# Kernel tuning notes

Measured on AMD Instinct MI355X. Metric: run time of the kernel, lower is better.

The kernel has to match this reference:

```python
import jax, jax.numpy as jnp
import numpy as np
from jax import lax

B, N, S, P, FIN, FFUT, H, NB, TOPK = 4, 1437, 56, 28, 10, 6, 64, 2, 5


def layer_norm(x, g, b, eps=1e-5):
    m = x.mean(-1, keepdims=True)
    v = ((x - m) ** 2).mean(-1, keepdims=True)
    return (x - m) * lax.rsqrt(v + eps) * g + b


def conv1d_same(x, w, pl, pr):
    # x: [BNF, 1, S], w: [1, 1, k]; torch Conv1d is cross-correlation == XLA conv
    return lax.conv_general_dilated(x, w, (1,), [(pl, pr)], dimension_numbers=('NCH', 'OIH', 'NCH'))


def gelu(x):
    return jax.nn.gelu(x, approximate=False)


def mixer_block(x, adj, wk, mk, lcg, lcb, ltg, ltb, lfg, lfb, lsg, lsb, tw, tb, fw, fb, sw, sb):
    Bx, Nx, Sx, Fx = x.shape
    # conv branch (pre-norm)
    xn = layer_norm(x, lcg, lcb)
    xc = xn.transpose(0, 1, 3, 2).reshape(Bx * Nx * Fx, 1, Sx)
    weekly = conv1d_same(xc, wk, 3, 3).reshape(Bx, Nx, Fx, Sx).transpose(0, 1, 3, 2)
    monthly = conv1d_same(xc, mk, 13, 14).reshape(Bx, Nx, Fx, Sx).transpose(0, 1, 3, 2)
    x = x + weekly + monthly
    # temporal MLP over S
    xn = layer_norm(x, ltg, ltb)
    xt = gelu(jnp.einsum('bnfs,os->bnfo', xn.transpose(0, 1, 3, 2), tw) + tb)
    x = x + xt.transpose(0, 1, 3, 2)
    # feature MLP over Feat
    xn = layer_norm(x, lfg, lfb)
    x = x + gelu(jnp.einsum('bnsf,of->bnso', xn, fw) + fb)
    # spatial propagation via dense bmm with adj
    xn = layer_norm(x, lsg, lsb)
    xp = jnp.einsum('bnsf,of->bnso', xn, sw).reshape(Bx, Nx, Sx * Fx)
    xs = jnp.einsum('bmn,bnd->bmd', adj, xp).reshape(Bx, Nx, Sx, Fx) + sb
    return x + xs


def reference(x, x_future, adj, fp_w, fp_b, in_ln_g, in_ln_b, q_w, q_b, k_w, k_b,
              node_emb, graph_alpha, blk_weekly, blk_monthly,
              blk_lnc_g, blk_lnc_b, blk_lnt_g, blk_lnt_b, blk_lnf_g, blk_lnf_b,
              blk_lns_g, blk_lns_b, blk_temp_w, blk_temp_b, blk_feat_w, blk_feat_b,
              blk_spat_w, blk_spat_b, futr_w, futr_b, head_w, head_b):
    Bx, Nx, Sx, _ = x.shape
    h = jnp.einsum('bnsf,hf->bnsh', x, fp_w) + fp_b
    h = layer_norm(h, in_ln_g, in_ln_b)
    emb = node_emb / jnp.maximum(jnp.linalg.norm(node_emb, axis=-1, keepdims=True), 1e-12)
    h = h + emb[None, :, None, :]
    # recency-weighted context
    decay = jnp.exp(-jnp.arange(Sx, 0, -1, dtype=jnp.float32) / 14.0)
    rw = decay / decay.sum()
    ctx = (h * rw[None, None, :, None]).sum(2)  # [B,N,H]
    Q = ctx @ q_w.T + q_b
    K = ctx @ k_w.T + k_b
    da = jnp.einsum('bnh,bmh->bnm', Q, K) / jnp.sqrt(jnp.float32(Q.shape[-1]))
    da = jax.nn.relu(jnp.clip(da, -10.0, 10.0))
    _, ti = lax.top_k(da, TOPK)
    mask = jax.vmap(jax.vmap(lambda row, idx: row.at[idx].set(1.0)))(
        jnp.zeros((Bx, Nx, Nx), da.dtype), ti)
    dyn = jax.nn.softmax(jnp.where(mask > 0, da, -jnp.inf), axis=2)
    dyn = jnp.nan_to_num(dyn)
    alpha = jax.nn.sigmoid(graph_alpha)  # shape (1,), broadcasts
    comb = alpha * adj[None, :, :] + (1.0 - alpha) * dyn
    comb = comb / jnp.maximum(jnp.abs(comb).sum(axis=2, keepdims=True), 1e-12)
    for i in range(NB):
        h = mixer_block(h, comb, blk_weekly[i], blk_monthly[i],
                        blk_lnc_g[i], blk_lnc_b[i], blk_lnt_g[i], blk_lnt_b[i],
                        blk_lnf_g[i], blk_lnf_b[i], blk_lns_g[i], blk_lns_b[i],
                        blk_temp_w[i], blk_temp_b[i], blk_feat_w[i], blk_feat_b[i],
                        blk_spat_w[i], blk_spat_b[i])
    hist = h.reshape(Bx, Nx, -1)
    fut = (jnp.einsum('bnpf,hf->bnph', x_future, futr_w) + futr_b).reshape(Bx, Nx, -1)
    feats = jnp.concatenate([hist, fut], axis=2)
    return feats @ head_w.T + head_b


def setup_inputs() -> dict:
    key = jax.random.key(0)
    ks = jax.random.split(key, 16)
    rn = lambda k, shp, s=1.0: jax.random.normal(k, shp, dtype=jnp.float32) * s
    return {
        'x': rn(ks[0], (B, N, S, FIN)),
        'x_future': rn(ks[1], (B, N, P, FFUT)),
        'adj': jax.random.uniform(ks[2], (N, N), dtype=jnp.float32),
        'fp_w': rn(ks[3], (H, FIN), 0.1), 'fp_b': jnp.zeros((H,), jnp.float32),
        'in_ln_g': jnp.ones((H,), jnp.float32), 'in_ln_b': jnp.zeros((H,), jnp.float32),
        'q_w': rn(ks[4], (H, H), 0.1), 'q_b': jnp.zeros((H,), jnp.float32),
        'k_w': rn(ks[5], (H, H), 0.1), 'k_b': jnp.zeros((H,), jnp.float32),
        'node_emb': rn(ks[6], (N, H), 0.02),
        'graph_alpha': jnp.full((1,), 2.2, jnp.float32),
        'blk_weekly': rn(ks[7], (NB, 1, 1, 7), 0.1),
        'blk_monthly': rn(ks[8], (NB, 1, 1, 28), 0.1),
        'blk_lnc_g': jnp.ones((NB, H), jnp.float32), 'blk_lnc_b': jnp.zeros((NB, H), jnp.float32),
        'blk_lnt_g': jnp.ones((NB, H), jnp.float32), 'blk_lnt_b': jnp.zeros((NB, H), jnp.float32),
        'blk_lnf_g': jnp.ones((NB, H), jnp.float32), 'blk_lnf_b': jnp.zeros((NB, H), jnp.float32),
        'blk_lns_g': jnp.ones((NB, H), jnp.float32), 'blk_lns_b': jnp.zeros((NB, H), jnp.float32),
        'blk_temp_w': rn(ks[9], (NB, S, S), 0.1), 'blk_temp_b': jnp.zeros((NB, S), jnp.float32),
        'blk_feat_w': rn(ks[10], (NB, H, H), 0.1), 'blk_feat_b': jnp.zeros((NB, H), jnp.float32),
        'blk_spat_w': rn(ks[11], (NB, H, H), 0.1), 'blk_spat_b': jnp.zeros((NB, H), jnp.float32),
        'futr_w': rn(ks[12], (H, FFUT), 0.1), 'futr_b': jnp.zeros((H,), jnp.float32),
        'head_w': rn(ks[13], (P, S * H + P * H), 0.02), 'head_b': jnp.zeros((P,), jnp.float32),
    }
```

## Files before the change

kernel.cpp:

```cpp
#include <hip/hip_runtime.h>
#include <hip/hip_bf16.h>
#include <math.h>

#define BB 4
#define NN 1437
#define SS 56
#define PP 28
#define FIN 10
#define FFUT 6
#define HH 64
#define NBLK 2
#define TOPK 5
#define DD (SS*HH)
#define FD (PP*HH)
#define TOT (DD+FD)
#define MP 1536
#define KP 1472
#define NT (KP/32)
#define WIMG_SZ 16384

typedef __attribute__((ext_vector_type(8))) __bf16 bf16x8;
typedef __attribute__((ext_vector_type(4))) float  f32x4;


__device__ __forceinline__ float gelu_fast(float x){
    float x2 = x*x;
    float u  = __builtin_fmaf(0.044715f*x2, x, x);
    float e  = __builtin_amdgcn_exp2f(2.3022077f*u);
    float r  = __builtin_amdgcn_rcpf(e+1.f);
    return x - x*r;
}
template<int C>
__device__ __forceinline__ float dppadd(float v){
    int x = __builtin_amdgcn_mov_dpp(__float_as_int(v), C, 0xF, 0xF, true);
    return v + __int_as_float(x);
}
__device__ __forceinline__ float row16_sum(float v){
    v = dppadd<0xB1>(v);
    v = dppadd<0x4E>(v);
    v = dppadd<0x141>(v);
    v = dppadd<0x140>(v);
    return v;
}
__device__ __forceinline__ float wave_sum64(float v){
    v = row16_sum(v);
    v += __shfl_xor(v,16,64);
    v += __shfl_xor(v,32,64);
    return v;
}
__device__ __forceinline__ void async_load16(const void* g, void* l){
    __builtin_amdgcn_global_load_lds(
        (const __attribute__((address_space(1))) void*)g,
        (__attribute__((address_space(3))) void*)l, 16, 0, 0);
}
__device__ __forceinline__ unsigned short f2bf(float x){
    unsigned int u = __float_as_uint(x);
    unsigned int r = (u + 0x7fffu + ((u>>16)&1u)) >> 16;
    return (unsigned short)r;
}
__device__ __forceinline__ float bf2f(unsigned short u){
    return __uint_as_float(((unsigned int)u)<<16);
}
__device__ __forceinline__ unsigned long long umax64(unsigned long long a, unsigned long long b){return a>b?a:b;}
__device__ __forceinline__ unsigned long long umin64(unsigned long long a, unsigned long long b){return a<b?a:b;}

#define INS5(a0,a1,a2,a3,a4,x) do{ unsigned long long t_=(x); \
    unsigned long long n0_=umax64(a0,t_), t1_=umin64(a0,t_); \
    unsigned long long n1_=umax64(a1,t1_), t2_=umin64(a1,t1_); \
    unsigned long long n2_=umax64(a2,t2_), t3_=umin64(a2,t2_); \
    unsigned long long n3_=umax64(a3,t3_), t4_=umin64(a3,t3_); \
    unsigned long long n4_=umax64(a4,t4_); \
    a0=n0_;a1=n1_;a2=n2_;a3=n3_;a4=n4_; }while(0)

#define MERGE5(a0,a1,a2,a3,a4,b0,b1,b2,b3,b4) do{ \
    unsigned long long o0_=umax64(a0,(b0)); \
    unsigned long long o1_=umax64(umax64((b1),umin64(a0,(b0))),a1); \
    unsigned long long o2_=umax64(umax64((b2),umin64(a0,(b1))),umax64(umin64(a1,(b0)),a2)); \
    unsigned long long o3_=umax64(umax64((b3),umin64(a0,(b2))),umax64(umin64(a1,(b1)),umax64(umin64(a2,(b0)),a3))); \
    unsigned long long o4_=umax64(umax64((b4),umin64(a0,(b3))),umax64(umax64(umin64(a1,(b2)),umin64(a2,(b1))),umax64(umin64(a3,(b0)),a4))); \
    a0=o0_;a1=o1_;a2=o2_;a3=o3_;a4=o4_; }while(0)

__global__ __launch_bounds__(256) void k_front(
    const float* __restrict__ x, const float* __restrict__ fpw, const float* __restrict__ fpb,
    const float* __restrict__ lng, const float* __restrict__ lnb,
    const float* __restrict__ nemb,
    const float* __restrict__ qw, const float* __restrict__ qb,
    const float* __restrict__ kw, const float* __restrict__ kb,
    float* __restrict__ h,
    unsigned short* __restrict__ qpack, unsigned short* __restrict__ kpack)
{
    int bn = blockIdx.x; int n = bn % NN;
    int tid=threadIdx.x; int lane=tid&63; int wv=tid>>6;
    __shared__ float xin[SS*FIN];
    __shared__ float wlds[HH*FIN];
    __shared__ float rw[SS];
    __shared__ float rsum;
    __shared__ float red[4][HH];
    __shared__ float ctxs[HH];
    for (int i=tid;i<SS*FIN;i+=256) xin[i]=x[(size_t)bn*SS*FIN+i];
    for (int i=tid;i<HH*FIN;i+=256) wlds[i]=fpw[i];
    if (tid<SS) rw[tid]=expf(-(float)(SS-tid)/14.0f);
    __syncthreads();
    if (tid==0){ float s=0.f; for(int i=0;i<SS;++i) s+=rw[i]; rsum=s; }
    __syncthreads();
    float inv_rs = 1.0f/rsum;
    float ev = nemb[(size_t)n*HH+lane];
    float ss = wave_sum64(ev*ev);
    float el = ev / fmaxf(sqrtf(ss), 1e-12f);
    float gg=lng[lane], bv=lnb[lane], fb0=fpb[lane];
    int paddr = (lane&15)*4 + (lane>>4);
    float cacc=0.f;
    for (int s=wv;s<SS;s+=4){
        float v=fb0;
        #pragma unroll
        for (int c=0;c<FIN;++c) v += xin[s*FIN+c]*wlds[lane*FIN+c];
        float m = wave_sum64(v)*(1.f/HH);
        float d = v-m;
        float va = wave_sum64(d*d)*(1.f/HH);
        float hn = d*rsqrtf(va+1e-5f)*gg + bv + el;
        h[((size_t)bn*SS+s)*HH + paddr]=hn;
        cacc += hn * rw[s]*inv_rs;
    }
    red[wv][lane]=cacc;
    __syncthreads();
    if (wv==0) ctxs[lane]=red[0][lane]+red[1][lane]+red[2][lane]+red[3][lane];
    __syncthreads();
    if (wv==0){
        const float4* qr = reinterpret_cast<const float4*>(qw + (size_t)lane*HH);
        const float4* kr = reinterpret_cast<const float4*>(kw + (size_t)lane*HH);
        float q=qb[lane], k=kb[lane];
        #pragma unroll 4
        for (int t=0;t<16;++t){
            float4 qv=qr[t], kv=kr[t];
            float c0=ctxs[4*t], c1=ctxs[4*t+1], c2=ctxs[4*t+2], c3=ctxs[4*t+3];
            q += qv.x*c0+qv.y*c1+qv.z*c2+qv.w*c3;
            k += kv.x*c0+kv.y*c1+kv.z*c2+kv.w*c3;
        }
        int b = bn/NN, m = bn%NN;
        size_t off = (size_t)b*8*MP*8 + (size_t)(lane>>3)*MP*8 + (size_t)m*8 + (lane&7);
        qpack[off]=f2bf(q); kpack[off]=f2bf(k);
    }
}

__global__ __launch_bounds__(256) void k_adjsum(
    const float* __restrict__ adj, float* __restrict__ adjsum)
{
    int m = blockIdx.x*4 + (threadIdx.x>>6);
    int lane = threadIdx.x & 63;
    if (m >= NN) return;
    const float* row = adj + (size_t)m*NN;
    float s=0.f;
    for (int n=lane;n<NN;n+=64) s += row[n];
    s = wave_sum64(s);
    if (lane==0) adjsum[m]=s;
}

__global__ __launch_bounds__(256) void k_qkt_top5(
    const unsigned short* __restrict__ qp, const unsigned short* __restrict__ kp,
    const float* __restrict__ adjsum, const float* __restrict__ galpha,
    int* __restrict__ meta_idx, float* __restrict__ meta_p, float* __restrict__ meta_inv)
{
    int m0 = blockIdx.x*32; int b = blockIdx.y;
    int tid=threadIdx.x, lane=tid&63, w=tid>>6;
    int g=lane>>4, c15=lane&15;
    int wr=w>>1, wc=w&1;
    __shared__ unsigned long long mls[64][5];

    const unsigned short* qb2 = qp + (size_t)b*8*MP*8;
    const unsigned short* kb2 = kp + (size_t)b*8*MP*8;
    bf16x8 af0 = *(const bf16x8*)(qb2 + ((size_t)(0*4+g)*MP + m0+wr*16+c15)*8);
    bf16x8 af1 = *(const bf16x8*)(qb2 + ((size_t)(1*4+g)*MP + m0+wr*16+c15)*8);

    unsigned long long A0=0,A1=0,A2=0,A3=0,A4=0;
    unsigned long long B0=0,B1=0,B2=0,B3=0,B4=0;
    unsigned long long C0=0,C1=0,C2=0,C3=0,C4=0;
    unsigned long long D0=0,D1=0,D2=0,D3=0,D4=0;

    for (int t=0;t<12;++t){
        int n0 = t*128;
        f32x4 acc[4];
        #pragma unroll
        for (int j=0;j<4;++j) acc[j]=(f32x4){0.f,0.f,0.f,0.f};
        #pragma unroll
        for (int j=0;j<4;++j){
            bf16x8 b0 = *(const bf16x8*)(kb2 + ((size_t)(0*4+g)*MP + n0+wc*64+j*16+c15)*8);
            bf16x8 b1 = *(const bf16x8*)(kb2 + ((size_t)(1*4+g)*MP + n0+wc*64+j*16+c15)*8);
            acc[j]=__builtin_amdgcn_mfma_f32_16x16x32_bf16(af0,b0,acc[j],0,0,0);
            acc[j]=__builtin_amdgcn_mfma_f32_16x16x32_bf16(af1,b1,acc[j],0,0,0);
        }
        #pragma unroll
        for (int j=0;j<4;++j){
            int n = n0 + wc*64 + j*16 + c15;
            bool ok = (n < NN);
            unsigned int lowk = 0xFFFFFFFFu - (unsigned)n;
            #define MKKEY(Q) ({ \
                float v_ = acc[j][Q]*0.125f; \
                v_ = fminf(fmaxf(v_,0.f),10.f); \
                ok ? (((unsigned long long)__float_as_uint(v_)<<32)|(unsigned long long)lowk) : 0ULL; })
            { unsigned long long k_=MKKEY(0); INS5(A0,A1,A2,A3,A4,k_); }
            { unsigned long long k_=MKKEY(1); INS5(B0,B1,B2,B3,B4,k_); }
            { unsigned long long k_=MKKEY(2); INS5(C0,C1,C2,C3,C4,k_); }
            { unsigned long long k_=MKKEY(3); INS5(D0,D1,D2,D3,D4,k_); }
            #undef MKKEY
        }
    }
    #pragma unroll
    for (int off=1; off<16; off<<=1){
        unsigned long long t0,t1,t2,t3,t4;
        t0=__shfl_xor(A0,off,64); t1=__shfl_xor(A1,off,64); t2=__shfl_xor(A2,off,64); t3=__shfl_xor(A3,off,64); t4=__shfl_xor(A4,off,64);
        MERGE5(A0,A1,A2,A3,A4,t0,t1,t2,t3,t4);
        t0=__shfl_xor(B0,off,64); t1=__shfl_xor(B1,off,64); t2=__shfl_xor(B2,off,64); t3=__shfl_xor(B3,off,64); t4=__shfl_xor(B4,off,64);
        MERGE5(B0,B1,B2,B3,B4,t0,t1,t2,t3,t4);
        t0=__shfl_xor(C0,off,64); t1=__shfl_xor(C1,off,64); t2=__shfl_xor(C2,off,64); t3=__shfl_xor(C3,off,64); t4=__shfl_xor(C4,off,64);
        MERGE5(C0,C1,C2,C3,C4,t0,t1,t2,t3,t4);
        t0=__shfl_xor(D0,off,64); t1=__shfl_xor(D1,off,64); t2=__shfl_xor(D2,off,64); t3=__shfl_xor(D3,off,64); t4=__shfl_xor(D4,off,64);
        MERGE5(D0,D1,D2,D3,D4,t0,t1,t2,t3,t4);
    }
    if (c15==0){
        int rb = wr*16 + g*4;
        mls[(rb+0)*2+wc][0]=A0; mls[(rb+0)*2+wc][1]=A1; mls[(rb+0)*2+wc][2]=A2; mls[(rb+0)*2+wc][3]=A3; mls[(rb+0)*2+wc][4]=A4;
        mls[(rb+1)*2+wc][0]=B0; mls[(rb+1)*2+wc][1]=B1; mls[(rb+1)*2+wc][2]=B2; mls[(rb+1)*2+wc][3]=B3; mls[(rb+1)*2+wc][4]=B4;
        mls[(rb+2)*2+wc][0]=C0; mls[(rb+2)*2+wc][1]=C1; mls[(rb+2)*2+wc][2]=C2; mls[(rb+2)*2+wc][3]=C3; mls[(rb+2)*2+wc][4]=C4;
        mls[(rb+3)*2+wc][0]=D0; mls[(rb+3)*2+wc][1]=D1; mls[(rb+3)*2+wc][2]=D2; mls[(rb+3)*2+wc][3]=D3; mls[(rb+3)*2+wc][4]=D4;
    }
    __syncthreads();
    if (tid < 32){
        int m = m0 + tid;
        if (m < NN){
            unsigned long long u0=mls[tid*2][0],u1=mls[tid*2][1],u2=mls[tid*2][2],u3=mls[tid*2][3],u4=mls[tid*2][4];
            MERGE5(u0,u1,u2,u3,u4, mls[tid*2+1][0],mls[tid*2+1][1],mls[tid*2+1][2],mls[tid*2+1][3],mls[tid*2+1][4]);
            float s0=__uint_as_float((unsigned)(u0>>32)), s1=__uint_as_float((unsigned)(u1>>32)),
                  s2=__uint_as_float((unsigned)(u2>>32)), s3=__uint_as_float((unsigned)(u3>>32)),
                  s4=__uint_as_float((unsigned)(u4>>32));
            int i0=(int)(0xFFFFFFFFu-(unsigned)u0), i1=(int)(0xFFFFFFFFu-(unsigned)u1),
                i2=(int)(0xFFFFFFFFu-(unsigned)u2), i3=(int)(0xFFFFFFFFu-(unsigned)u3),
                i4=(int)(0xFFFFFFFFu-(unsigned)u4);
            float e0=1.f, e1=expf(s1-s0), e2=expf(s2-s0), e3=expf(s3-s0), e4=expf(s4-s0);
            float den=e0+e1+e2+e3+e4;
            float alpha=1.f/(1.f+expf(-galpha[0]));
            float oma=(1.f-alpha)/den;
            size_t base = ((size_t)b*NN + m)*5;
            meta_idx[base+0]=i0; meta_idx[base+1]=i1; meta_idx[base+2]=i2; meta_idx[base+3]=i3; meta_idx[base+4]=i4;
            meta_p[base+0]=oma*e0; meta_p[base+1]=oma*e1; meta_p[base+2]=oma*e2; meta_p[base+3]=oma*e3; meta_p[base+4]=oma*e4;
            meta_inv[(size_t)b*NN+m] = 1.f/fmaxf(alpha*adjsum[m] + (1.f-alpha), 1e-12f);
        }
    }
}

__global__ __launch_bounds__(256) void k_blend(
    const float* __restrict__ adj, const float* __restrict__ galpha,
    const int* __restrict__ meta_idx, const float* __restrict__ meta_p,
    const float* __restrict__ meta_inv, __hip_bfloat16* __restrict__ combh)
{
    int m=blockIdx.x, b=blockIdx.y, tid=threadIdx.x;
    size_t base = ((size_t)b*NN + m)*5;
    int i0=meta_idx[base+0], i1=meta_idx[base+1], i2=meta_idx[base+2],
        i3=meta_idx[base+3], i4=meta_idx[base+4];
    float p0=meta_p[base+0], p1=meta_p[base+1], p2=meta_p[base+2],
          p3=meta_p[base+3], p4=meta_p[base+4];
    float inv = meta_inv[(size_t)b*NN+m];
    float alpha=1.f/(1.f+expf(-galpha[0]));
    const float* arow = adj + (size_t)m*NN;
    __hip_bfloat16* dst = combh + ((size_t)b*MP+m)*KP;
    float ai = alpha*inv;
    for (int n=tid;n<KP;n+=256){
        float v = 0.f;
        if (n<NN){
            v = ai*arow[n];
            v += (n==i0)?p0*inv:0.f;
            v += (n==i1)?p1*inv:0.f;
            v += (n==i2)?p2*inv:0.f;
            v += (n==i3)?p3*inv:0.f;
            v += (n==i4)?p4*inv:0.f;
        }
        dst[n]=__float2bfloat16(v);
    }
}

__global__ __launch_bounds__(256) void k_prepw(
    const float* __restrict__ wk, const float* __restrict__ mk,
    const float* __restrict__ tw, const float* __restrict__ fw,
    const float* __restrict__ sw, unsigned short* __restrict__ wimg)
{
    int i = blockIdx.x; int tid = threadIdx.x;
    const float* wki = wk + i*7;
    const float* mki = mk + i*28;
    const float* twi = tw + i*SS*SS;
    const float* fwi = fw + i*HH*HH;
    const float* swi = sw + i*HH*HH;
    unsigned short* o = wimg + (size_t)i*WIMG_SZ;
    for (int e=tid; e<4096; e+=256){
        int r = e>>6, k = e&63;
        int swz = ((k*2) ^ ((r&7)<<4)) >> 1;
        float mv = 0.f;
        if (r<SS && k<SS){
            int a = k-r+3;  if (a>=0 && a<7)  mv += wki[a];
            int b2= k-r+13; if (b2>=0 && b2<28) mv += mki[b2];
        }
        o[r*64 + swz] = f2bf(mv);
        float tv = (r<SS && k<SS) ? twi[r*SS+k] : 0.f;
        o[4096 + r*64 + swz] = f2bf(tv);
        int pk = (k>>3)*512 + r*8 + (k&7);
        o[8192  + pk] = f2bf(fwi[r*HH+k]);
        o[12288 + pk] = f2bf(swi[r*HH+k]);
    }
}

__global__ __launch_bounds__(256) void k_prep_head(
    const float* __restrict__ hw, __hip_bfloat16* __restrict__ hw16)
{
    int i = blockIdx.x*256 + threadIdx.x;
    int r = i / TOT, k = i - r*TOT;
    float v = (r<PP) ? hw[(size_t)r*TOT + k] : 0.f;
    hw16[i] = __float2bfloat16(v);
}

__global__ __launch_bounds__(256) void k_fut(
    const float* __restrict__ xf, const float* __restrict__ fw,
    const float* __restrict__ fbias, __hip_bfloat16* __restrict__ feats)
{
    int bn=blockIdx.x, tid=threadIdx.x;
    __shared__ float fwl[HH*FFUT];
    __shared__ float fbl[HH];
    __shared__ float xfl[PP*FFUT];
    for (int i=tid;i<HH*FFUT;i+=256) fwl[i]=fw[i];
    if (tid<HH) fbl[tid]=fbias[tid];
    for (int i=tid;i<PP*FFUT;i+=256) xfl[i]=xf[(size_t)bn*PP*FFUT+i];
    __syncthreads();
    __hip_bfloat16* dst = feats + (size_t)bn*TOT + DD;
    for (int q=tid;q<FD;q+=256){
        int pp=q>>6, hh2=q&63;
        float v=fbl[hh2];
        #pragma unroll
        for (int c2=0;c2<FFUT;++c2) v += xfl[pp*FFUT+c2]*fwl[hh2*FFUT+c2];
        dst[q]=__float2bfloat16(v);
    }
}

__global__ __launch_bounds__(256) void k_mixer2(
    float* __restrict__ h, unsigned short* __restrict__ xpg,
    const unsigned short* __restrict__ spat_in,
    const unsigned short* __restrict__ wimg,
    const float* __restrict__ lncg, const float* __restrict__ lncb,
    const float* __restrict__ lntg, const float* __restrict__ lntb,
    const float* __restrict__ lnfg, const float* __restrict__ lnfb,
    const float* __restrict__ lnsg, const float* __restrict__ lnsb,
    const float* __restrict__ tb, const float* __restrict__ fb)
{
    int bid = blockIdx.x;
    int xx = bid & 7, ii = bid >> 3;
    int bn = (xx < 4) ? xx*719 + ii : 2876 + (xx-4)*718 + ii;
    int tid=threadIdx.x, lane=tid&63, w=tid>>6;
    int g=lane>>4, c=lane&15;
    __shared__ unsigned short wbuf[2][4096];
    __shared__ unsigned short xs[4096];
    __shared__ float prm[640];

    const char* wsrc=(const char*)wimg;
#define LOADW(SLOTB, BUFP) do{ \
    async_load16(wsrc+(size_t)(SLOTB)+((size_t)tid)*16,       (char*)(BUFP)+(w*64)*16); \
    async_load16(wsrc+(size_t)(SLOTB)+((size_t)(256+tid))*16, (char*)(BUFP)+((256+w*64))*16); } while(0)

    LOADW(0,    wbuf[0]);
    LOADW(8192, wbuf[1]);
    if (tid<64){
        prm[tid]      =lncg[tid]; prm[64+tid] =lncb[tid];
        prm[128+tid]  =lntg[tid]; prm[192+tid]=lntb[tid];
        prm[256+tid]  =lnfg[tid]; prm[320+tid]=lnfb[tid];
        prm[384+tid]  =lnsg[tid]; prm[448+tid]=lnsb[tid];
        prm[512+tid]  =(tid<SS)?tb[tid]:0.f;
        prm[576+tid]  =fb[tid];
    }
    float xl[4][4];
    float* hb = h + (size_t)bn*DD;
    int srow = 16*w + 4*g;
    #pragma unroll
    for (int q=0;q<4;++q){
        int s=srow+q;
        if (s<SS){
            const float4 v4 = *reinterpret_cast<const float4*>(hb + s*HH + c*4);
            float a0=v4.x, a1=v4.y, a2=v4.z, a3=v4.w;
            if (spat_in){
                ushort4 sv = *reinterpret_cast<const ushort4*>(spat_in + (size_t)bn*TOT + s*HH + c*4);
                a0 += bf2f(sv.x); a1 += bf2f(sv.y); a2 += bf2f(sv.z); a3 += bf2f(sv.w);
            }
            xl[q][0]=a0; xl[q][1]=a1; xl[q][2]=a2; xl[q][3]=a3;
        } else {
            xl[q][0]=0.f; xl[q][1]=0.f; xl[q][2]=0.f; xl[q][3]=0.f;
        }
    }
    __syncthreads();

    float xn[4][4];
    f32x4 acc[4];

#define LNSTAGE(GOFF,BOFF) do{ \
    _Pragma("unroll") \
    for (int q=0;q<4;++q){ \
        float sv = xl[q][0]+xl[q][1]+xl[q][2]+xl[q][3]; \
        float s2 = xl[q][0]*xl[q][0]+xl[q][1]*xl[q][1]+xl[q][2]*xl[q][2]+xl[q][3]*xl[q][3]; \
        sv = row16_sum(sv); \
        s2 = row16_sum(s2); \
        float mn = sv*(1.f/64.f); \
        float var = s2*(1.f/64.f)-mn*mn; \
        float rstd = rsqrtf(var+1e-5f); \
        bool ok = (srow+q)<SS; \
        _Pragma("unroll") \
        for (int tj=0;tj<4;++tj){ \
            float v=(xl[q][tj]-mn)*rstd*prm[(GOFF)+tj*16+c]+prm[(BOFF)+tj*16+c]; \
            xn[q][tj]= ok ? v : 0.f; \
        } \
    } }while(0)

#define WRITE_XNP() do{ \
    _Pragma("unroll") \
    for (int qp=0;qp<2;++qp){ \
        int s0=srow+2*qp; \
        _Pragma("unroll") \
        for (int tj=0;tj<4;++tj){ \
            unsigned int pv=(unsigned int)f2bf(xn[2*qp][tj])|((unsigned int)f2bf(xn[2*qp+1][tj])<<16); \
            *(unsigned int*)((char*)xs + ((s0>>3)*1024 + (tj*16+c)*16 + (s0&7)*2)) = pv; \
        } \
    } }while(0)

#define WRITE_XNR() do{ \
    _Pragma("unroll") \
    for (int q=0;q<4;++q){ int s=srow+q; \
        _Pragma("unroll") \
        for (int tj=0;tj<4;++tj){ \
            *(unsigned short*)((char*)xs + s*128 + (((tj*16+c)*2) ^ ((s&7)<<4))) = f2bf(xn[q][tj]); \
        } \
    } }while(0)

#define MM(APTR,BPTR) do{ \
    _Pragma("unroll") \
    for (int tj=0;tj<4;++tj) acc[tj]=(f32x4){0.f,0.f,0.f,0.f}; \
    _Pragma("unroll") \
    for (int kc=0;kc<2;++kc){ \
        int arow=16*w+c; \
        bf16x8 af=*(const bf16x8*)((const char*)(APTR)+arow*128+((kc*64+g*16)^((arow&7)<<4))); \
        _Pragma("unroll") \
        for (int tj=0;tj<4;++tj){ \
            bf16x8 bf2=*(const bf16x8*)((const char*)(BPTR)+(kc*4+g)*1024+(tj*16+c)*16); \
            acc[tj]=__builtin_amdgcn_mfma_f32_16x16x32_bf16(af,bf2,acc[tj],0,0,0); \
        } \
    } }while(0)

    LNSTAGE(0,64); WRITE_XNP();
    __syncthreads();
    MM(&wbuf[0][0], xs);
    #pragma unroll
    for (int q=0;q<4;++q)
        #pragma unroll
        for (int tj=0;tj<4;++tj) xl[q][tj]+=acc[tj][q];
    __syncthreads();
    LOADW(16384, wbuf[0]);
    LNSTAGE(128,192); WRITE_XNP();
    __syncthreads();
    MM(&wbuf[1][0], xs);
    #pragma unroll
    for (int q=0;q<4;++q){
        float tbv=prm[512+srow+q];
        #pragma unroll
        for (int tj=0;tj<4;++tj) xl[q][tj]+=gelu_fast(acc[tj][q]+tbv);
    }
    __syncthreads();
    LOADW(24576, wbuf[1]);
    LNSTAGE(256,320); WRITE_XNR();
    __syncthreads();
    MM(xs, &wbuf[0][0]);
    #pragma unroll
    for (int q=0;q<4;++q)
        #pragma unroll
        for (int tj=0;tj<4;++tj) xl[q][tj]+=gelu_fast(acc[tj][q]+prm[576+tj*16+c]);
    __syncthreads();
    LNSTAGE(384,448); WRITE_XNR();
    __syncthreads();
    MM(xs, &wbuf[1][0]);
    int b_=bn/NN, n_=bn%NN;
    unsigned short* xpo = xpg + ((size_t)b_*(KP/8) + (size_t)(n_>>3))*(size_t)DD*8 + (n_&7);
    #pragma unroll
    for (int q=0;q<4;++q){
        int s=srow+q;
        if (s<SS){
            float4 hv; hv.x=xl[q][0]; hv.y=xl[q][1]; hv.z=xl[q][2]; hv.w=xl[q][3];
            *reinterpret_cast<float4*>(hb + s*HH + c*4) = hv;
            #pragma unroll
            for (int tj=0;tj<4;++tj){
                int d = s*HH + tj*16 + c;
                xpo[(size_t)d*8] = f2bf(acc[tj][q]);
            }
        }
    }
#undef LNSTAGE
#undef WRITE_XNP
#undef WRITE_XNR
#undef MM
#undef LOADW
}

__global__ __launch_bounds__(256,4) void k_bmm_mfma(
    const __hip_bfloat16* __restrict__ combh,
    const __hip_bfloat16* __restrict__ xpg,
    const float* __restrict__ sb,
    const float* __restrict__ h,
    unsigned short* __restrict__ spat_out,
    __hip_bfloat16* __restrict__ feats_out)
{
    __shared__ short As[3][2048];
    __shared__ short Bs[3][4096];

    int bid = blockIdx.x;
    int wg = (bid & 7)*336 + (bid >> 3);
    int bm = wg % 24; int tmp2 = wg / 24; int bd = tmp2 % 28; int b = tmp2 / 28;
    int tid=threadIdx.x, lane=tid&63, w=tid>>6;
    int g=lane>>4, c=lane&15;
    int wr=w>>1, wc=w&1;
    int m0=bm*64, d0=bd*128;

    const char* cb = (const char*)(combh + (size_t)b*MP*KP);
    const char* xb = (const char*)(xpg   + (size_t)b*(KP/8)*(size_t)DD*8);

    int arow_s = tid>>2, aslot = tid&3;
    int ag = aslot ^ ((arow_s>>1)&3);
    const char* srcA = cb + ((size_t)(m0+arow_s)*KP + ag*8)*2;
    int bch = tid>>7, bcol = tid&127;
    const char* srcB0 = xb + ((size_t)bch*DD + d0 + bcol)*16;
    const char* srcB1 = xb + ((size_t)(bch+2)*DD + d0 + bcol)*16;
    const size_t BSTEP = (size_t)4*DD*16;

    f32x4 acc[2][4];
    #pragma unroll
    for (int i=0;i<2;++i)
        #pragma unroll
        for (int j=0;j<4;++j) acc[i][j]=(f32x4){0.f,0.f,0.f,0.f};

    int aoff[2], boff[4];
    #pragma unroll
    for (int i=0;i<2;++i){
        int row = 32*wr + 16*i + c;
        aoff[i] = row*64 + ((g*16) ^ (((row>>1)&3)<<4));
    }
    #pragma unroll
    for (int j=0;j<4;++j) boff[j] = (g*128 + 64*wc + 16*j + c)*16;

#define STAGE(BUF,T) do { \
    async_load16(srcA  + (size_t)(T)*64,    (char*)As[BUF] + w*1024); \
    async_load16(srcB0 + (size_t)(T)*BSTEP, (char*)Bs[BUF] + w*1024); \
    async_load16(srcB1 + (size_t)(T)*BSTEP, (char*)Bs[BUF] + 4096 + w*1024); } while(0)

    STAGE(0,0); STAGE(1,1);
    asm volatile("s_waitcnt vmcnt(3)" ::: "memory");
    __builtin_amdgcn_s_barrier();

    int cur=0;
    for (int t=0;t<NT;++t){
        if (t+2<NT){
            int nb = cur+2; if (nb>=3) nb-=3;
            STAGE(nb, t+2);
        }
        const char* Ab=(const char*)As[cur];
        const char* Bb=(const char*)Bs[cur];
        bf16x8 af[2], bfv[4];
        #pragma unroll
        for (int i=0;i<2;++i) af[i]=*(const bf16x8*)(Ab + aoff[i]);
        #pragma unroll
        for (int j=0;j<4;++j) bfv[j]=*(const bf16x8*)(Bb + boff[j]);
        #pragma unroll
        for (int i=0;i<2;++i)
            #pragma unroll
            for (int j=0;j<4;++j)
                acc[i][j]=__builtin_amdgcn_mfma_f32_16x16x32_bf16(af[i],bfv[j],acc[i][j],0,0,0);
        if (t+2<NT) asm volatile("s_waitcnt vmcnt(3)" ::: "memory");
        else        asm volatile("s_waitcnt vmcnt(0)" ::: "memory");
        __builtin_amdgcn_s_barrier();
        ++cur; if (cur>=3) cur=0;
    }
#undef STAGE

    int row_b = m0 + 32*wr + g*4;
    int s2 = 2*bd + wc;
    float sb0=sb[c], sb1=sb[16+c], sb2=sb[32+c], sb3=sb[48+c];
    #pragma unroll
    for (int i=0;i<2;++i){
        #pragma unroll
        for (int q=0;q<4;++q){
            int m = row_b + 16*i + q;
            if (m < NN){
                if (spat_out){
                    ushort4 pv;
                    pv.x = f2bf(acc[i][0][q] + sb0);
                    pv.y = f2bf(acc[i][1][q] + sb1);
                    pv.z = f2bf(acc[i][2][q] + sb2);
                    pv.w = f2bf(acc[i][3][q] + sb3);
                    *reinterpret_cast<ushort4*>(spat_out + ((size_t)b*NN+m)*TOT + s2*HH + c*4) = pv;
                } else {
                    const float* hp = h + ((size_t)b*NN+m)*DD + s2*HH + c*4;
                    float4 hv = *reinterpret_cast<const float4*>(hp);
                    float nv0 = hv.x + acc[i][0][q] + sb0;
                    float nv1 = hv.y + acc[i][1][q] + sb1;
                    float nv2 = hv.z + acc[i][2][q] + sb2;
                    float nv3 = hv.w + acc[i][3][q] + sb3;
                    size_t fr = ((size_t)b*NN+m)*TOT + (size_t)bd*128 + wc*64;
                    feats_out[fr + c]      = __float2bfloat16(nv0);
                    feats_out[fr + 16 + c] = __float2bfloat16(nv1);
                    feats_out[fr + 32 + c] = __float2bfloat16(nv2);
                    feats_out[fr + 48 + c] = __float2bfloat16(nv3);
                }
            }
        }
    }
}

__global__ __launch_bounds__(256) void k_head_mfma(
    const __hip_bfloat16* __restrict__ feats, const __hip_bfloat16* __restrict__ hw16,
    const float* __restrict__ hb, float* __restrict__ out)
{
    int tid=threadIdx.x, lane=tid&63, w=tid>>6;
    int g=lane>>4, c=lane&15;
    int m0=blockIdx.x*32;
    int rt=w>>1, pt=w&1;
    int arow = m0 + rt*16 + c;
    if (arow > BB*NN-1) arow = BB*NN-1;
    const char* abase = (const char*)feats + (size_t)arow*TOT*2 + g*16;
    const char* bbase = (const char*)hw16 + (size_t)(pt*16+c)*TOT*2 + g*16;
    f32x4 acc=(f32x4){0.f,0.f,0.f,0.f};
    #pragma unroll 4
    for (int kc=0;kc<TOT/32;++kc){
        bf16x8 af =*(const bf16x8*)(abase + (size_t)kc*64);
        bf16x8 bf2=*(const bf16x8*)(bbase + (size_t)kc*64);
        acc=__builtin_amdgcn_mfma_f32_16x16x32_bf16(af,bf2,acc,0,0,0);
    }
    int col = pt*16 + c;
    #pragma unroll
    for (int q=0;q<4;++q){
        int row = m0 + rt*16 + g*4 + q;
        if (row < BB*NN && col < PP)
            out[(size_t)row*PP + col] = acc[q] + hb[col];
    }
}

extern "C" void kernel_launch(void* const* d_in, const int* in_sizes, int n_in,
                              void* d_out, int out_size, void* d_ws, size_t ws_size,
                              hipStream_t stream)
{
    const float* x      = (const float*)d_in[0];
    const float* xfut   = (const float*)d_in[1];
    const float* adj    = (const float*)d_in[2];
    const float* fp_w   = (const float*)d_in[3];
    const float* fp_b   = (const float*)d_in[4];
    const float* inlng  = (const float*)d_in[5];
    const float* inlnb  = (const float*)d_in[6];
    const float* q_w    = (const float*)d_in[7];
    const float* q_b    = (const float*)d_in[8];
    const float* k_w    = (const float*)d_in[9];
    const float* k_b    = (const float*)d_in[10];
    const float* nemb   = (const float*)d_in[11];
    const float* galpha = (const float*)d_in[12];
    const float* wk     = (const float*)d_in[13];
    const float* mk     = (const float*)d_in[14];
    const float* lncg   = (const float*)d_in[15];
    const float* lncb   = (const float*)d_in[16];
    const float* lntg   = (const float*)d_in[17];
    const float* lntb   = (const float*)d_in[18];
    const float* lnfg   = (const float*)d_in[19];
    const float* lnfb   = (const float*)d_in[20];
    const float* lnsg   = (const float*)d_in[21];
    const float* lnsb   = (const float*)d_in[22];
    const float* tw     = (const float*)d_in[23];
    const float* tb     = (const float*)d_in[24];
    const float* fw     = (const float*)d_in[25];
    const float* fb     = (const float*)d_in[26];
    const float* sw     = (const float*)d_in[27];
    const float* sb     = (const float*)d_in[28];
    const float* futw   = (const float*)d_in[29];
    const float* futb   = (const float*)d_in[30];
    const float* hw     = (const float*)d_in[31];
    const float* hb     = (const float*)d_in[32];
    (void)in_sizes; (void)n_in; (void)out_size; (void)ws_size;
    float* out = (float*)d_out;
    float* ws = (float*)d_ws;
    const size_t HSZ = (size_t)BB*NN*SS*HH;

    float* h    = ws;
    __hip_bfloat16* combh = (__hip_bfloat16*)(h + HSZ);
    __hip_bfloat16* xpg   = combh + (size_t)BB*MP*KP;
    unsigned short* wimg  = (unsigned short*)(xpg + (size_t)BB*(KP/8)*(size_t)DD*8);
    unsigned short* qpack = wimg + (size_t)NBLK*WIMG_SZ;
    unsigned short* kpack = qpack + (size_t)BB*8*MP*8;
    __hip_bfloat16* feats16 = (__hip_bfloat16*)(kpack + (size_t)BB*8*MP*8);
    __hip_bfloat16* hw16    = feats16 + (size_t)BB*NN*TOT;
    float* adjsum   = (float*)(hw16 + (size_t)32*TOT);
    int*   meta_idx = (int*)(adjsum + NN);
    float* meta_p   = (float*)(meta_idx + (size_t)BB*NN*5);
    float* meta_inv = meta_p + (size_t)BB*NN*5;

    k_prepw<<<NBLK,256,0,stream>>>(wk, mk, tw, fw, sw, wimg);
    k_prep_head<<<(32*TOT)/256,256,0,stream>>>(hw, hw16);
    k_adjsum<<<(NN+3)/4,256,0,stream>>>(adj, adjsum);
    k_fut<<<BB*NN,256,0,stream>>>(xfut, futw, futb, feats16);
    k_front<<<BB*NN,256,0,stream>>>(x, fp_w, fp_b, inlng, inlnb, nemb,
                                    q_w,q_b,k_w,k_b, h, qpack, kpack);
    dim3 gq5(MP/32, BB);
    k_qkt_top5<<<gq5,256,0,stream>>>(qpack, kpack, adjsum, galpha,
                                     meta_idx, meta_p, meta_inv);
    dim3 gbl(NN, BB);
    k_blend<<<gbl,256,0,stream>>>(adj, galpha, meta_idx, meta_p, meta_inv, combh);
    for (int b2=0;b2<BB;++b2)
        hipMemsetAsync(xpg + ((size_t)b2*(KP/8)+179)*(size_t)DD*8, 0,
                       (size_t)5*DD*8*sizeof(__hip_bfloat16), stream);
    k_mixer2<<<BB*NN,256,0,stream>>>(h, (unsigned short*)xpg, (const unsigned short*)nullptr,
        wimg, lncg,lncb, lntg,lntb, lnfg,lnfb, lnsg,lnsb, tb, fb);
    k_bmm_mfma<<<2688,256,0,stream>>>(combh, xpg, sb, h,
        (unsigned short*)feats16, (__hip_bfloat16*)nullptr);
    k_mixer2<<<BB*NN,256,0,stream>>>(h, (unsigned short*)xpg, (const unsigned short*)feats16,
        wimg + WIMG_SZ, lncg+HH,lncb+HH, lntg+HH,lntb+HH, lnfg+HH,lnfb+HH, lnsg+HH,lnsb+HH,
        tb+SS, fb+HH);
    k_bmm_mfma<<<2688,256,0,stream>>>(combh, xpg, sb+HH, h,
        (unsigned short*)nullptr, feats16);
    k_head_mfma<<<(BB*NN+31)/32,256,0,stream>>>(feats16, hw16, hb, out);
}
```

Measured before the change: 515.6 us.

## Run the adjacency bmm in FP8 with per-row normalization applied in the epilogue

The blended adjacency matrix and the projected activations are now stored as FP8 (e4m3) instead of bf16, and the spatial bmm uses the fp8 MFMA instruction with a reworked LDS staging layout and higher occupancy hint. The per-row normalization factor is moved out of the blend and applied in the bmm epilogue, so the stored fp8 values have a better range. This halves the bytes moved for the dominant bmm operands and raises MFMA throughput. The cost is reduced precision in the spatial propagation, which may hurt accuracy against the reference.

Measured after the change: 598.8 us. 1.16x slower.

```diff
diff --git a/kernel.cpp b/kernel.cpp
--- a/kernel.cpp
+++ b/kernel.cpp
@@ -16,11 +16,13 @@
 #define TOT (DD+FD)
 #define MP 1536
 #define KP 1472
+#define KC8 (KP/8)
 #define NT (KP/32)
 #define WIMG_SZ 16384
 
 typedef __attribute__((ext_vector_type(8))) __bf16 bf16x8;
 typedef __attribute__((ext_vector_type(4))) float  f32x4;
+typedef unsigned long long u64;
 
 
 __device__ __forceinline__ float gelu_fast(float x){
@@ -53,6 +55,11 @@
         (const __attribute__((address_space(1))) void*)g,
         (__attribute__((address_space(3))) void*)l, 16, 0, 0);
 }
+__device__ __forceinline__ void async_load4(const void* g, void* l){
+    __builtin_amdgcn_global_load_lds(
+        (const __attribute__((address_space(1))) void*)g,
+        (__attribute__((address_space(3))) void*)l, 4, 0, 0);
+}
 __device__ __forceinline__ unsigned short f2bf(float x){
     unsigned int u = __float_as_uint(x);
     unsigned int r = (u + 0x7fffu + ((u>>16)&1u)) >> 16;
@@ -61,23 +68,30 @@
 __device__ __forceinline__ float bf2f(unsigned short u){
     return __uint_as_float(((unsigned int)u)<<16);
 }
-__device__ __forceinline__ unsigned long long umax64(unsigned long long a, unsigned long long b){return a>b?a:b;}
-__device__ __forceinline__ unsigned long long umin64(unsigned long long a, unsigned long long b){return a<b?a:b;}
-
-#define INS5(a0,a1,a2,a3,a4,x) do{ unsigned long long t_=(x); \
-    unsigned long long n0_=umax64(a0,t_), t1_=umin64(a0,t_); \
-    unsigned long long n1_=umax64(a1,t1_), t2_=umin64(a1,t1_); \
-    unsigned long long n2_=umax64(a2,t2_), t3_=umin64(a2,t2_); \
-    unsigned long long n3_=umax64(a3,t3_), t4_=umin64(a3,t3_); \
-    unsigned long long n4_=umax64(a4,t4_); \
+__device__ __forceinline__ unsigned char f2fp8(float x){
+    return (unsigned char)(__builtin_amdgcn_cvt_pk_fp8_f32(x, 0.f, 0, false) & 0xFF);
+}
+__device__ __forceinline__ unsigned int pack4fp8(float a, float b, float c, float d){
+    int lo = __builtin_amdgcn_cvt_pk_fp8_f32(a, b, 0, false);
+    return (unsigned int)__builtin_amdgcn_cvt_pk_fp8_f32(c, d, lo, true);
+}
+__device__ __forceinline__ u64 umax64(u64 a, u64 b){return a>b?a:b;}
+__device__ __forceinline__ u64 umin64(u64 a, u64 b){return a<b?a:b;}
+
+#define INS5(a0,a1,a2,a3,a4,x) do{ u64 t_=(x); \
+    u64 n0_=umax64(a0,t_), t1_=umin64(a0,t_); \
+    u64 n1_=umax64(a1,t1_), t2_=umin64(a1,t1_); \
+    u64 n2_=umax64(a2,t2_), t3_=umin64(a2,t2_); \
+    u64 n3_=umax64(a3,t3_), t4_=umin64(a3,t3_); \
+    u64 n4_=umax64(a4,t4_); \
     a0=n0_;a1=n1_;a2=n2_;a3=n3_;a4=n4_; }while(0)
 
 #define MERGE5(a0,a1,a2,a3,a4,b0,b1,b2,b3,b4) do{ \
-    unsigned long long o0_=umax64(a0,(b0)); \
-    unsigned long long o1_=umax64(umax64((b1),umin64(a0,(b0))),a1); \
-    unsigned long long o2_=umax64(umax64((b2),umin64(a0,(b1))),umax64(umin64(a1,(b0)),a2)); \
-    unsigned long long o3_=umax64(umax64((b3),umin64(a0,(b2))),umax64(umin64(a1,(b1)),umax64(umin64(a2,(b0)),a3))); \
-    unsigned long long o4_=umax64(umax64((b4),umin64(a0,(b3))),umax64(umax64(umin64(a1,(b2)),umin64(a2,(b1))),umax64(umin64(a3,(b0)),a4))); \
+    u64 o0_=umax64(a0,(b0)); \
+    u64 o1_=umax64(umax64((b1),umin64(a0,(b0))),a1); \
+    u64 o2_=umax64(umax64((b2),umin64(a0,(b1))),umax64(umin64(a1,(b0)),a2)); \
+    u64 o3_=umax64(umax64((b3),umin64(a0,(b2))),umax64(umin64(a1,(b1)),umax64(umin64(a2,(b0)),a3))); \
+    u64 o4_=umax64(umax64((b4),umin64(a0,(b3))),umax64(umax64(umin64(a1,(b2)),umin64(a2,(b1))),umax64(umin64(a3,(b0)),a4))); \
     a0=o0_;a1=o1_;a2=o2_;a3=o3_;a4=o4_; }while(0)
 
 __global__ __launch_bounds__(256) void k_front(
@@ -164,17 +178,17 @@
     int tid=threadIdx.x, lane=tid&63, w=tid>>6;
     int g=lane>>4, c15=lane&15;
     int wr=w>>1, wc=w&1;
-    __shared__ unsigned long long mls[64][5];
+    __shared__ u64 mls[64][5];
 
     const unsigned short* qb2 = qp + (size_t)b*8*MP*8;
     const unsigned short* kb2 = kp + (size_t)b*8*MP*8;
     bf16x8 af0 = *(const bf16x8*)(qb2 + ((size_t)(0*4+g)*MP + m0+wr*16+c15)*8);
     bf16x8 af1 = *(const bf16x8*)(qb2 + ((size_t)(1*4+g)*MP + m0+wr*16+c15)*8);
 
-    unsigned long long A0=0,A1=0,A2=0,A3=0,A4=0;
-    unsigned long long B0=0,B1=0,B2=0,B3=0,B4=0;
-    unsigned long long C0=0,C1=0,C2=0,C3=0,C4=0;
-    unsigned long long D0=0,D1=0,D2=0,D3=0,D4=0;
+    u64 A0=0,A1=0,A2=0,A3=0,A4=0;
+    u64 B0=0,B1=0,B2=0,B3=0,B4=0;
+    u64 C0=0,C1=0,C2=0,C3=0,C4=0;
+    u64 D0=0,D1=0,D2=0,D3=0,D4=0;
 
     for (int t=0;t<12;++t){
         int n0 = t*128;
@@ -196,17 +210,17 @@
             #define MKKEY(Q) ({ \
                 float v_ = acc[j][Q]*0.125f; \
                 v_ = fminf(fmaxf(v_,0.f),10.f); \
-                ok ? (((unsigned long long)__float_as_uint(v_)<<32)|(unsigned long long)lowk) : 0ULL; })
-            { unsigned long long k_=MKKEY(0); INS5(A0,A1,A2,A3,A4,k_); }
-            { unsigned long long k_=MKKEY(1); INS5(B0,B1,B2,B3,B4,k_); }
-            { unsigned long long k_=MKKEY(2); INS5(C0,C1,C2,C3,C4,k_); }
-            { unsigned long long k_=MKKEY(3); INS5(D0,D1,D2,D3,D4,k_); }
+                ok ? (((u64)__float_as_uint(v_)<<32)|(u64)lowk) : 0ULL; })
+            { u64 k_=MKKEY(0); INS5(A0,A1,A2,A3,A4,k_); }
+            { u64 k_=MKKEY(1); INS5(B0,B1,B2,B3,B4,k_); }
+            { u64 k_=MKKEY(2); INS5(C0,C1,C2,C3,C4,k_); }
+            { u64 k_=MKKEY(3); INS5(D0,D1,D2,D3,D4,k_); }
             #undef MKKEY
         }
     }
     #pragma unroll
     for (int off=1; off<16; off<<=1){
-        unsigned long long t0,t1,t2,t3,t4;
+        u64 t0,t1,t2,t3,t4;
         t0=__shfl_xor(A0,off,64); t1=__shfl_xor(A1,off,64); t2=__shfl_xor(A2,off,64); t3=__shfl_xor(A3,off,64); t4=__shfl_xor(A4,off,64);
         MERGE5(A0,A1,A2,A3,A4,t0,t1,t2,t3,t4);
         t0=__shfl_xor(B0,off,64); t1=__shfl_xor(B1,off,64); t2=__shfl_xor(B2,off,64); t3=__shfl_xor(B3,off,64); t4=__shfl_xor(B4,off,64);
@@ -227,7 +241,7 @@
     if (tid < 32){
         int m = m0 + tid;
         if (m < NN){
-            unsigned long long u0=mls[tid*2][0],u1=mls[tid*2][1],u2=mls[tid*2][2],u3=mls[tid*2][3],u4=mls[tid*2][4];
+            u64 u0=mls[tid*2][0],u1=mls[tid*2][1],u2=mls[tid*2][2],u3=mls[tid*2][3],u4=mls[tid*2][4];
             MERGE5(u0,u1,u2,u3,u4, mls[tid*2+1][0],mls[tid*2+1][1],mls[tid*2+1][2],mls[tid*2+1][3],mls[tid*2+1][4]);
             float s0=__uint_as_float((unsigned)(u0>>32)), s1=__uint_as_float((unsigned)(u1>>32)),
                   s2=__uint_as_float((unsigned)(u2>>32)), s3=__uint_as_float((unsigned)(u3>>32)),
@@ -250,7 +264,7 @@
 __global__ __launch_bounds__(256) void k_blend(
     const float* __restrict__ adj, const float* __restrict__ galpha,
     const int* __restrict__ meta_idx, const float* __restrict__ meta_p,
-    const float* __restrict__ meta_inv, __hip_bfloat16* __restrict__ combh)
+    unsigned char* __restrict__ comb8)
 {
     int m=blockIdx.x, b=blockIdx.y, tid=threadIdx.x;
     size_t base = ((size_t)b*NN + m)*5;
@@ -258,22 +272,26 @@
         i3=meta_idx[base+3], i4=meta_idx[base+4];
     float p0=meta_p[base+0], p1=meta_p[base+1], p2=meta_p[base+2],
           p3=meta_p[base+3], p4=meta_p[base+4];
-    float inv = meta_inv[(size_t)b*NN+m];
     float alpha=1.f/(1.f+expf(-galpha[0]));
     const float* arow = adj + (size_t)m*NN;
-    __hip_bfloat16* dst = combh + ((size_t)b*MP+m)*KP;
-    float ai = alpha*inv;
-    for (int n=tid;n<KP;n+=256){
-        float v = 0.f;
-        if (n<NN){
-            v = ai*arow[n];
-            v += (n==i0)?p0*inv:0.f;
-            v += (n==i1)?p1*inv:0.f;
-            v += (n==i2)?p2*inv:0.f;
-            v += (n==i3)?p3*inv:0.f;
-            v += (n==i4)?p4*inv:0.f;
-        }
-        dst[n]=__float2bfloat16(v);
+    unsigned char* dst = comb8 + ((size_t)b*MP+m)*KP;
+    for (int n4=tid; n4<KP/4; n4+=256){
+        float v[4];
+        #pragma unroll
+        for (int k=0;k<4;++k){
+            int n = n4*4+k;
+            float vv = 0.f;
+            if (n<NN){
+                vv = alpha*arow[n];
+                vv += (n==i0)?p0:0.f;
+                vv += (n==i1)?p1:0.f;
+                vv += (n==i2)?p2:0.f;
+                vv += (n==i3)?p3:0.f;
+                vv += (n==i4)?p4:0.f;
+            }
+            v[k]=vv;
+        }
+        *reinterpret_cast<unsigned int*>(dst + n4*4) = pack4fp8(v[0],v[1],v[2],v[3]);
     }
 }
 
@@ -338,7 +356,7 @@
 }
 
 __global__ __launch_bounds__(256) void k_mixer2(
-    float* __restrict__ h, unsigned short* __restrict__ xpg,
+    float* __restrict__ h, unsigned char* __restrict__ xpg8,
     const unsigned short* __restrict__ spat_in,
     const unsigned short* __restrict__ wimg,
     const float* __restrict__ lncg, const float* __restrict__ lncb,
@@ -478,7 +496,7 @@
     __syncthreads();
     MM(xs, &wbuf[1][0]);
     int b_=bn/NN, n_=bn%NN;
-    unsigned short* xpo = xpg + ((size_t)b_*(KP/8) + (size_t)(n_>>3))*(size_t)DD*8 + (n_&7);
+    unsigned char* xpo = xpg8 + ((size_t)b_*KC8 + (size_t)(n_>>3))*(size_t)DD*8 + (n_&7);
     #pragma unroll
     for (int q=0;q<4;++q){
         int s=srow+q;
@@ -488,7 +506,7 @@
             #pragma unroll
             for (int tj=0;tj<4;++tj){
                 int d = s*HH + tj*16 + c;
-                xpo[(size_t)d*8] = f2bf(acc[tj][q]);
+                xpo[(size_t)d*8] = f2fp8(acc[tj][q]);
             }
         }
     }
@@ -499,16 +517,18 @@
 #undef LOADW
 }
 
-__global__ __launch_bounds__(256,4) void k_bmm_mfma(
-    const __hip_bfloat16* __restrict__ combh,
-    const __hip_bfloat16* __restrict__ xpg,
+__global__ __launch_bounds__(256,8) void k_bmm_mfma(
+    const unsigned char* __restrict__ comb8,
+    const unsigned char* __restrict__ xpg8,
     const float* __restrict__ sb,
     const float* __restrict__ h,
+    const float* __restrict__ meta_inv,
     unsigned short* __restrict__ spat_out,
     __hip_bfloat16* __restrict__ feats_out)
 {
-    __shared__ short As[3][2048];
-    __shared__ short Bs[3][4096];
+    __shared__ unsigned char As8[3][2048];
+    __shared__ unsigned char Bs8[3][4096];
+    __shared__ float sinv[64];
 
     int bid = blockIdx.x;
     int wg = (bid & 7)*336 + (bid >> 3);
@@ -518,16 +538,22 @@
     int wr=w>>1, wc=w&1;
     int m0=bm*64, d0=bd*128;
 
-    const char* cb = (const char*)(combh + (size_t)b*MP*KP);
-    const char* xb = (const char*)(xpg   + (size_t)b*(KP/8)*(size_t)DD*8);
-
-    int arow_s = tid>>2, aslot = tid&3;
-    int ag = aslot ^ ((arow_s>>1)&3);
-    const char* srcA = cb + ((size_t)(m0+arow_s)*KP + ag*8)*2;
-    int bch = tid>>7, bcol = tid&127;
-    const char* srcB0 = xb + ((size_t)bch*DD + d0 + bcol)*16;
-    const char* srcB1 = xb + ((size_t)(bch+2)*DD + d0 + bcol)*16;
-    const size_t BSTEP = (size_t)4*DD*16;
+    const unsigned char* cb = comb8 + (size_t)b*MP*KP;
+    const unsigned char* xb = xpg8  + (size_t)b*KC8*(size_t)DD*8;
+
+    int ch0 = tid, ch1 = 256 + tid;
+    int r0=(ch0>>1)&63, h0=ch0&1, kl0=ch0>>7;
+    int r1=(ch1>>1)&63, h1=ch1&1, kl1=ch1>>7;
+    const unsigned char* srcA0 = cb + (size_t)(m0+r0)*KP + kl0*8 + h0*4;
+    const unsigned char* srcA1 = cb + (size_t)(m0+r1)*KP + kl1*8 + h1*4;
+    int klB = tid>>6, dpair = tid&63;
+    const unsigned char* srcB = xb + ((size_t)klB*DD + d0 + dpair*2)*8;
+    const size_t BSTEP = (size_t)4*DD*8;
+
+    if (tid < 64){
+        int m = m0 + tid;
+        sinv[tid] = (m < NN) ? meta_inv[(size_t)b*NN + m] : 0.f;
+    }
 
     f32x4 acc[2][4];
     #pragma unroll
@@ -537,20 +563,17 @@
 
     int aoff[2], boff[4];
     #pragma unroll
-    for (int i=0;i<2;++i){
-        int row = 32*wr + 16*i + c;
-        aoff[i] = row*64 + ((g*16) ^ (((row>>1)&3)<<4));
-    }
-    #pragma unroll
-    for (int j=0;j<4;++j) boff[j] = (g*128 + 64*wc + 16*j + c)*16;
+    for (int i=0;i<2;++i) aoff[i] = g*512 + (32*wr + 16*i + c)*8;
+    #pragma unroll
+    for (int j=0;j<4;++j) boff[j] = g*1024 + (64*wc + 16*j + c)*8;
 
 #define STAGE(BUF,T) do { \
-    async_load16(srcA  + (size_t)(T)*64,    (char*)As[BUF] + w*1024); \
-    async_load16(srcB0 + (size_t)(T)*BSTEP, (char*)Bs[BUF] + w*1024); \
-    async_load16(srcB1 + (size_t)(T)*BSTEP, (char*)Bs[BUF] + 4096 + w*1024); } while(0)
+    async_load4 (srcA0 + (size_t)(T)*32,    (char*)As8[BUF] + tid*4); \
+    async_load4 (srcA1 + (size_t)(T)*32,    (char*)As8[BUF] + 1024 + tid*4); \
+    async_load16(srcB  + (size_t)(T)*BSTEP, (char*)Bs8[BUF] + tid*16); } while(0)
 
     STAGE(0,0); STAGE(1,1);
-    asm volatile("s_waitcnt vmcnt(3)" ::: "memory");
+    asm volatile("s_waitcnt vmcnt(3) lgkmcnt(0)" ::: "memory");
     __builtin_amdgcn_s_barrier();
 
     int cur=0;
@@ -559,18 +582,18 @@
             int nb = cur+2; if (nb>=3) nb-=3;
             STAGE(nb, t+2);
         }
-        const char* Ab=(const char*)As[cur];
-        const char* Bb=(const char*)Bs[cur];
-        bf16x8 af[2], bfv[4];
-        #pragma unroll
-        for (int i=0;i<2;++i) af[i]=*(const bf16x8*)(Ab + aoff[i]);
-        #pragma unroll
-        for (int j=0;j<4;++j) bfv[j]=*(const bf16x8*)(Bb + boff[j]);
+        const char* Ab=(const char*)As8[cur];
+        const char* Bb=(const char*)Bs8[cur];
+        u64 af[2], bfv[4];
+        #pragma unroll
+        for (int i=0;i<2;++i) af[i]=*(const u64*)(Ab + aoff[i]);
+        #pragma unroll
+        for (int j=0;j<4;++j) bfv[j]=*(const u64*)(Bb + boff[j]);
         #pragma unroll
         for (int i=0;i<2;++i)
             #pragma unroll
             for (int j=0;j<4;++j)
-                acc[i][j]=__builtin_amdgcn_mfma_f32_16x16x32_bf16(af[i],bfv[j],acc[i][j],0,0,0);
+                acc[i][j]=__builtin_amdgcn_mfma_f32_16x16x32_fp8_fp8((long)af[i],(long)bfv[j],acc[i][j],0,0,0);
         if (t+2<NT) asm volatile("s_waitcnt vmcnt(3)" ::: "memory");
         else        asm volatile("s_waitcnt vmcnt(0)" ::: "memory");
         __builtin_amdgcn_s_barrier();
@@ -587,20 +610,21 @@
         for (int q=0;q<4;++q){
             int m = row_b + 16*i + q;
             if (m < NN){
+                float inv = sinv[32*wr + g*4 + 16*i + q];
                 if (spat_out){
                     ushort4 pv;
-                    pv.x = f2bf(acc[i][0][q] + sb0);
-                    pv.y = f2bf(acc[i][1][q] + sb1);
-                    pv.z = f2bf(acc[i][2][q] + sb2);
-                    pv.w = f2bf(acc[i][3][q] + sb3);
+                    pv.x = f2bf(inv*acc[i][0][q] + sb0);
+                    pv.y = f2bf(inv*acc[i][1][q] + sb1);
+                    pv.z = f2bf(inv*acc[i][2][q] + sb2);
+                    pv.w = f2bf(inv*acc[i][3][q] + sb3);
                     *reinterpret_cast<ushort4*>(spat_out + ((size_t)b*NN+m)*TOT + s2*HH + c*4) = pv;
                 } else {
                     const float* hp = h + ((size_t)b*NN+m)*DD + s2*HH + c*4;
                     float4 hv = *reinterpret_cast<const float4*>(hp);
-                    float nv0 = hv.x + acc[i][0][q] + sb0;
-                    float nv1 = hv.y + acc[i][1][q] + sb1;
-                    float nv2 = hv.z + acc[i][2][q] + sb2;
-                    float nv3 = hv.w + acc[i][3][q] + sb3;
+                    float nv0 = hv.x + inv*acc[i][0][q] + sb0;
+                    float nv1 = hv.y + inv*acc[i][1][q] + sb1;
+                    float nv2 = hv.z + inv*acc[i][2][q] + sb2;
+                    float nv3 = hv.w + inv*acc[i][3][q] + sb3;
                     size_t fr = ((size_t)b*NN+m)*TOT + (size_t)bd*128 + wc*64;
                     feats_out[fr + c]      = __float2bfloat16(nv0);
                     feats_out[fr + 16 + c] = __float2bfloat16(nv1);
@@ -682,10 +706,10 @@
     float* ws = (float*)d_ws;
     const size_t HSZ = (size_t)BB*NN*SS*HH;
 
-    float* h    = ws;
-    __hip_bfloat16* combh = (__hip_bfloat16*)(h + HSZ);
-    __hip_bfloat16* xpg   = combh + (size_t)BB*MP*KP;
-    unsigned short* wimg  = (unsigned short*)(xpg + (size_t)BB*(KP/8)*(size_t)DD*8);
+    float* h = ws;
+    unsigned char* comb8 = (unsigned char*)(h + HSZ);
+    unsigned char* xpg8  = comb8 + (size_t)BB*MP*KP;
+    unsigned short* wimg  = (unsigned short*)(xpg8 + (size_t)BB*KC8*(size_t)DD*8);
     unsigned short* qpack = wimg + (size_t)NBLK*WIMG_SZ;
     unsigned short* kpack = qpack + (size_t)BB*8*MP*8;
     __hip_bfloat16* feats16 = (__hip_bfloat16*)(kpack + (size_t)BB*8*MP*8);
@@ -705,18 +729,18 @@
     k_qkt_top5<<<gq5,256,0,stream>>>(qpack, kpack, adjsum, galpha,
                                      meta_idx, meta_p, meta_inv);
     dim3 gbl(NN, BB);
-    k_blend<<<gbl,256,0,stream>>>(adj, galpha, meta_idx, meta_p, meta_inv, combh);
+    k_blend<<<gbl,256,0,stream>>>(adj, galpha, meta_idx, meta_p, comb8);
     for (int b2=0;b2<BB;++b2)
-        hipMemsetAsync(xpg + ((size_t)b2*(KP/8)+179)*(size_t)DD*8, 0,
-                       (size_t)5*DD*8*sizeof(__hip_bfloat16), stream);
-    k_mixer2<<<BB*NN,256,0,stream>>>(h, (unsigned short*)xpg, (const unsigned short*)nullptr,
+        hipMemsetAsync(xpg8 + ((size_t)b2*KC8+179)*(size_t)DD*8, 0,
+                       (size_t)5*DD*8, stream);
+    k_mixer2<<<BB*NN,256,0,stream>>>(h, xpg8, (const unsigned short*)nullptr,
         wimg, lncg,lncb, lntg,lntb, lnfg,lnfb, lnsg,lnsb, tb, fb);
-    k_bmm_mfma<<<2688,256,0,stream>>>(combh, xpg, sb, h,
+    k_bmm_mfma<<<2688,256,0,stream>>>(comb8, xpg8, sb, h, meta_inv,
         (unsigned short*)feats16, (__hip_bfloat16*)nullptr);
-    k_mixer2<<<BB*NN,256,0,stream>>>(h, (unsigned short*)xpg, (const unsigned short*)feats16,
+    k_mixer2<<<BB*NN,256,0,stream>>>(h, xpg8, (const unsigned short*)feats16,
         wimg + WIMG_SZ, lncg+HH,lncb+HH, lntg+HH,lntb+HH, lnfg+HH,lnfb+HH, lnsg+HH,lnsb+HH,
         tb+SS, fb+HH);
-    k_bmm_mfma<<<2688,256,0,stream>>>(combh, xpg, sb+HH, h,
+    k_bmm_mfma<<<2688,256,0,stream>>>(comb8, xpg8, sb+HH, h, meta_inv,
         (unsigned short*)nullptr, feats16);
     k_head_mfma<<<(BB*NN+31)/32,256,0,stream>>>(feats16, hw16, hb, out);
 }
```
